# Kernel tuning notes

Measured on AMD Instinct MI355X. Metric: run time of the kernel, lower is better.

## Reference

```python
import jax, jax.numpy as jnp
import numpy as np

EPS = 1e-5
COMMIT_W = 2.0
LATENT = 64


def _conv1d(x, w, b, stride, padding):
    # x: [B,C,T], w: [O,I,K] (torch Conv1d layout)
    y = jax.lax.conv_general_dilated(x, w, (stride,), [(padding, padding)],
                                     dimension_numbers=('NCH', 'OIH', 'NCH'))
    return y + b[None, :, None]


def _bn(x, g, b):
    # training-mode BatchNorm1d: batch statistics over (B, T) per channel
    mu = x.mean(axis=(0, 2), keepdims=True)
    var = x.var(axis=(0, 2), keepdims=True)
    return (x - mu) * jax.lax.rsqrt(var + EPS) * g[None, :, None] + b[None, :, None]


def setup_inputs():
    key = jax.random.key(0)
    ks = jax.random.split(key, 10)
    B, T, D, K = 8, 10240, LATENT, 8192
    f32 = jnp.float32
    def n(k, shape, scale):
        return jax.random.normal(k, shape, dtype=f32) * scale
    return {
        'x': jax.random.normal(ks[0], (B, 1, T), dtype=f32),
        'enc_w1': n(ks[1], (16, 1, 5), 0.3), 'enc_b1': jnp.zeros((16,), f32),
        'bn1_g': jnp.ones((16,), f32), 'bn1_b': jnp.zeros((16,), f32),
        'enc_w2': n(ks[2], (32, 16, 5), 0.1), 'enc_b2': jnp.zeros((32,), f32),
        'bn2_g': jnp.ones((32,), f32), 'bn2_b': jnp.zeros((32,), f32),
        'enc_w3': n(ks[3], (64, 32, 25), 0.05), 'enc_b3': jnp.zeros((64,), f32),
        'bn3_g': jnp.ones((64,), f32), 'bn3_b': jnp.zeros((64,), f32),
        'codebook': jax.random.normal(ks[4], (K, D), dtype=f32),
        'dec_wt': n(ks[5], (64, 64, 25), 0.05),  # torch ConvTranspose1d [in,out,k]
        'dbn1_g': jnp.ones((64,), f32), 'dbn1_b': jnp.zeros((64,), f32),
        'dec_w2': n(ks[6], (64, 64, 5), 0.08), 'dec_b2': jnp.zeros((64,), f32),
        'dbn2_g': jnp.ones((64,), f32), 'dbn2_b': jnp.zeros((64,), f32),
        'dec_w3': n(ks[7], (1, 64, 1), 0.1), 'dec_b3': jnp.zeros((1,), f32),
    }


def reference(x, enc_w1, enc_b1, bn1_g, bn1_b, enc_w2, enc_b2, bn2_g, bn2_b,
              enc_w3, enc_b3, bn3_g, bn3_b, codebook, dec_wt, dbn1_g, dbn1_b,
              dec_w2, dec_b2, dbn2_g, dbn2_b, dec_w3, dec_b3):
    # ---- encoder ----
    h = jax.nn.silu(_conv1d(x, enc_w1, enc_b1, 1, 2))
    h = _bn(h, bn1_g, bn1_b)
    h = jax.nn.silu(_conv1d(h, enc_w2, enc_b2, 1, 2))
    h = _bn(h, bn2_g, bn2_b)
    h = jnp.tanh(_conv1d(h, enc_w3, enc_b3, 5, 12))
    z = _bn(h, bn3_g, bn3_b)                       # [B, 64, L]
    B, _, L = z.shape
    # ---- VQ: euclidean nearest-neighbor against codebook ----
    zf = z.transpose(0, 2, 1).reshape(-1, LATENT)  # [N, D]
    d = ((zf * zf).sum(-1, keepdims=True)
         - 2.0 * zf @ codebook.T
         + (codebook * codebook).sum(-1)[None, :])  # [N, K]
    idx = jnp.argmin(d, axis=-1)                   # [N]
    q = codebook[idx]                              # [N, D]
    commit_loss = COMMIT_W * jnp.mean((jax.lax.stop_gradient(q) - zf) ** 2)
    q_st = zf + jax.lax.stop_gradient(q - zf)      # straight-through
    zq = q_st.reshape(B, L, LATENT).transpose(0, 2, 1)  # [B, 64, L]
    # ---- decoder ----
    # ConvTranspose1d(k=25, s=5, p=12) == dilated conv with flipped kernel
    wconv = jnp.flip(dec_wt, -1).transpose(1, 0, 2)     # [out, in, k]
    h = jax.lax.conv_general_dilated(zq, wconv, (1,), [(12, 12)], lhs_dilation=(5,),
                                     dimension_numbers=('NCH', 'OIH', 'NCH'))
    h = jax.nn.silu(h)
    h = _bn(h, dbn1_g, dbn1_b)
    h = jax.nn.silu(_conv1d(h, dec_w2, dec_b2, 1, 2))
    h = _bn(h, dbn2_g, dbn2_b)
    recon = _conv1d(h, dec_w3, dec_b3, 1, 0)       # [B, 1, ~T]
    T = x.shape[2]
    cur = recon.shape[2]
    if cur > T:
        recon = recon[:, :, :T]
    elif cur < T:
        recon = jnp.pad(recon, ((0, 0), (0, 0), (0, T - cur)))
    return recon, idx.reshape(B, L), commit_loss
```

## Files before the change

kernel.cpp:

```cpp
#include <hip/hip_runtime.h>
#include <hip/hip_bf16.h>

#define DEV __device__ __forceinline__

typedef __attribute__((ext_vector_type(8))) short s8v;
typedef __attribute__((ext_vector_type(16))) float f32x16;
typedef __attribute__((address_space(1))) const unsigned int u32g;
typedef __attribute__((address_space(3))) unsigned int u32l;

DEV void gl_lds(const void* g, void* l){
  __builtin_amdgcn_global_load_lds((u32g*)g, (u32l*)l, 16, 0, 0);
}

DEV float siluf(float x){ return x / (1.f + expf(-x)); }

DEV float wredsum(float v){
  #pragma unroll
  for(int m = 32; m; m >>= 1) v += __shfl_xor(v, m);
  return v;
}

DEV unsigned short bf16rne(float f){
  unsigned int u = __float_as_uint(f);
  u += 0x7FFFu + ((u >> 16) & 1u);
  return (unsigned short)(u >> 16);
}
DEV float bf16tof(unsigned short h){ return __uint_as_float(((unsigned int)h) << 16); }

DEV unsigned umed3(unsigned a, unsigned b, unsigned c){
  unsigned d;
  asm("v_med3_u32 %0, %1, %2, %3" : "=v"(d) : "v"(a), "v"(b), "v"(c));
  return d;
}

#define S1 0
#define Q1 16
#define S2 32
#define Q2 64
#define S3 96
#define Q3 160
#define S4 224
#define Q4 288
#define S5 352
#define Q5 416
#define SLOSS 480
#define NSTATF 512

#define EPSQ 6u
#define NCHUNK 8

__global__ void k_prep(const float* dwt, unsigned short* wb7){
  const int n2 = 64*64*25;
  for(int j = blockIdx.x*blockDim.x + threadIdx.x; j < n2; j += gridDim.x*blockDim.x){
    int ii = j/(64*25), r = j - ii*(64*25), o = r/25, k = r - o*25;
    wb7[((size_t)(k*64 + o))*64 + ii] = bf16rne(dwt[j]);
  }
}

__global__ void k_prep2(const float* __restrict__ cb, unsigned short* __restrict__ cbsw,
                        float* __restrict__ cnw, float* __restrict__ cnw2,
                        unsigned short* __restrict__ cbb, int* cnt){
  if(blockIdx.x == 0 && threadIdx.x == 0) *cnt = 0;
  int j = blockIdx.x*256 + threadIdx.x;
  if(j < 8192){
    float nrm = 0.f;
    unsigned swz = (j & 15) << 4;
    char* rowp = (char*)cbsw + (size_t)j*256;
    #pragma unroll
    for(int k = 0; k < 64; k++){
      float x = cb[(size_t)j*64 + k];
      unsigned short hi = bf16rne(x);
      float lo = x - bf16tof(hi);
      *(unsigned short*)(rowp + (((unsigned)(2*k)) ^ swz)) = hi;
      *(unsigned short*)(rowp + (((unsigned)(128 + 2*k)) ^ swz)) = bf16rne(lo);
      cbb[(size_t)j*64 + k] = hi;
      nrm = fmaf(x, x, nrm);
    }
    cnw[j] = nrm;
    cnw2[j] = (nrm + 1024.f) * 256.f;
  }
}

__global__ void k1(const float* __restrict__ x, const float* __restrict__ w1,
                   const float* __restrict__ b1, float* __restrict__ h1, float* stats){
  __shared__ float xs[136];
  __shared__ float ssum[16], ssq[16];
  int tid = threadIdx.x, b = blockIdx.y, t0 = blockIdx.x*128;
  if(tid < 16){ ssum[tid] = 0.f; ssq[tid] = 0.f; }
  for(int i = tid; i < 132; i += 256){
    int t = t0 + i - 2;
    xs[i] = (t >= 0 && t < 10240) ? x[b*10240 + t] : 0.f;
  }
  __syncthreads();
  int c = tid & 15, sgrp = tid >> 4;
  float w[5];
  #pragma unroll
  for(int k = 0; k < 5; k++) w[k] = w1[c*5 + k];
  float bias = b1[c];
  float outv[8];
  float ps = 0.f, pq = 0.f;
  #pragma unroll
  for(int s = 0; s < 8; s++){
    float a = bias;
    #pragma unroll
    for(int k = 0; k < 5; k++) a = fmaf(w[k], xs[sgrp*8 + s + k], a);
    a = siluf(a);
    outv[s] = a;
    ps += a; pq += a*a;
  }
  float* op = h1 + ((size_t)(b*16 + c))*10240 + t0 + sgrp*8;
  #pragma unroll
  for(int q = 0; q < 2; q++)
    *(float4*)(op + q*4) = make_float4(outv[q*4], outv[q*4+1], outv[q*4+2], outv[q*4+3]);
  ps += __shfl_xor(ps, 16); pq += __shfl_xor(pq, 16);
  ps += __shfl_xor(ps, 32); pq += __shfl_xor(pq, 32);
  if((tid & 48) == 0){ atomicAdd(&ssum[c], ps); atomicAdd(&ssq[c], pq); }
  __syncthreads();
  if(tid < 16){ atomicAdd(stats+S1+tid, ssum[tid]); atomicAdd(stats+Q1+tid, ssq[tid]); }
}

__global__ __launch_bounds__(256) void k2(const float* __restrict__ h1,
                   const float* __restrict__ w2, const float* __restrict__ b2,
                   const float* __restrict__ g1, const float* __restrict__ bb1,
                   float* __restrict__ h2out, float* stats){
  __shared__ float hs[16][136];
  __shared__ float A1s[16], B1s[16];
  __shared__ float ssum[32], ssq[32];
  int tid = threadIdx.x, b = blockIdx.y, t0 = blockIdx.x*128;
  if(tid < 16){
    float mu = stats[S1+tid]/81920.f;
    float var = stats[Q1+tid]/81920.f - mu*mu;
    float rs = rsqrtf(var + 1e-5f);
    A1s[tid] = rs*g1[tid];
    B1s[tid] = bb1[tid] - mu*rs*g1[tid];
  }
  if(tid < 32){ ssum[tid] = 0.f; ssq[tid] = 0.f; }
  __syncthreads();
  {
    int ch = tid >> 4, j0 = tid & 15;
    float A = A1s[ch], B = B1s[ch];
    const float* hp = h1 + ((size_t)(b*16 + ch))*10240;
    for(int j = j0; j < 132; j += 16){
      int t = t0 + j - 2;
      hs[ch][j] = (t >= 0 && t < 10240) ? hp[t]*A + B : 0.f;
    }
  }
  __syncthreads();
  int c = tid & 31, tgrp = tid >> 5;
  int tb = tgrp*16;
  float acc[16];
  float bias = b2[c];
  #pragma unroll
  for(int s = 0; s < 16; s++) acc[s] = bias;
  for(int ic = 0; ic < 4; ic++){
    float wf[20];
    const float* wp = w2 + c*80 + ic*20;
    #pragma unroll
    for(int q = 0; q < 5; q++) *(float4*)(wf + q*4) = *(const float4*)(wp + q*4);
    #pragma unroll
    for(int di = 0; di < 4; di++){
      int i = ic*4 + di;
      float z[20];
      #pragma unroll
      for(int q = 0; q < 5; q++) *(float4*)(z + q*4) = *(const float4*)(&hs[i][tb] + q*4);
      float w0 = wf[di*5], w1 = wf[di*5+1], w2v = wf[di*5+2], w3 = wf[di*5+3], w4 = wf[di*5+4];
      #pragma unroll
      for(int s = 0; s < 16; s++)
        acc[s] = fmaf(w0, z[s], fmaf(w1, z[s+1], fmaf(w2v, z[s+2],
                 fmaf(w3, z[s+3], fmaf(w4, z[s+4], acc[s])))));
    }
  }
  float ps = 0.f, pq = 0.f;
  #pragma unroll
  for(int s = 0; s < 16; s++){
    float a = siluf(acc[s]);
    acc[s] = a;
    ps += a; pq += a*a;
  }
  float* op = h2out + ((size_t)(b*32 + c))*10240 + t0 + tb;
  #pragma unroll
  for(int q = 0; q < 4; q++)
    *(float4*)(op + q*4) = make_float4(acc[q*4], acc[q*4+1], acc[q*4+2], acc[q*4+3]);
  ps += __shfl_xor(ps, 32); pq += __shfl_xor(pq, 32);
  if((tid & 32) == 0){ atomicAdd(&ssum[c], ps); atomicAdd(&ssq[c], pq); }
  __syncthreads();
  if(tid < 32){ atomicAdd(stats+S2+tid, ssum[tid]); atomicAdd(stats+Q2+tid, ssq[tid]); }
}

__global__ void k3w(const float* __restrict__ ew3, const float* __restrict__ eb3,
                    const float* __restrict__ g2, const float* __restrict__ bb2,
                    const float* __restrict__ stats, float* __restrict__ w3f8,
                    float* __restrict__ cbias, float* __restrict__ zpad){
  __shared__ float A2[32], B2[32];
  __shared__ float red[256];
  int tid = threadIdx.x;
  if(tid < 32){
    float mu = stats[S2+tid]/81920.f;
    float var = stats[Q2+tid]/81920.f - mu*mu;
    float rs = rsqrtf(var + 1e-5f);
    A2[tid] = rs*g2[tid];
    B2[tid] = bb2[tid] - mu*rs*g2[tid];
  }
  __syncthreads();
  if(blockIdx.x < 200){
    int e = blockIdx.x*256 + tid;
    int kap = e % 5; int r = e / 5;
    int c = r & 63; r >>= 6;
    int kk = r % 5; int i = r / 5;
    float w = ew3[c*800 + i*25 + kap*5 + kk];
    w3f8[(((size_t)(i*5 + kk))*64 + c)*8 + kap] = w * A2[i];
  } else {
    if(tid < 32){
      float a = A2[tid];
      zpad[tid] = (fabsf(a) > 1e-30f) ? (-B2[tid] / a) : 0.f;
    }
    int c = tid & 63, ig = tid >> 6;
    float s = 0.f;
    for(int i = ig*8; i < ig*8 + 8; i++){
      float wsum = 0.f;
      #pragma unroll
      for(int k = 0; k < 25; k++) wsum += ew3[c*800 + i*25 + k];
      s += wsum * B2[i];
    }
    red[tid] = s;
    __syncthreads();
    if(tid < 64) cbias[tid] = eb3[tid] + red[tid] + red[tid+64] + red[tid+128] + red[tid+192];
  }
}

__global__ __launch_bounds__(256) void k3(const float* __restrict__ h2,
                   const float* __restrict__ w3f8, const float* __restrict__ cbias,
                   const float* __restrict__ zpad,
                   float* __restrict__ zn, float* stats){
  __shared__ float ssum[64], ssq[64];
  int tid = threadIdx.x, b = blockIdx.y, l0 = blockIdx.x*32;
  if(tid < 64){ ssum[tid] = 0.f; ssq[tid] = 0.f; }
  __syncthreads();
  int c = tid & 63, lslot = tid >> 6;
  int tbase = 5*(l0 + lslot*8) - 12;
  bool edge = (blockIdx.x == 0) || (blockIdx.x == 63);
  float acc[8];
  float cb0 = cbias[c];
  #pragma unroll
  for(int s = 0; s < 8; s++) acc[s] = cb0;
  for(int i = 0; i < 32; i++){
    const float* hp = h2 + ((size_t)(b*32 + i))*10240;
    float z[60];
    if(edge){
      float zp_i = zpad[i];
      #pragma unroll
      for(int e = 0; e < 60; e++){
        int t = tbase + e;
        z[e] = (t >= 0 && t < 10240) ? hp[t] : zp_i;
      }
    } else {
      #pragma unroll
      for(int q = 0; q < 15; q++)
        *(float4*)(z + q*4) = *(const float4*)(hp + tbase + q*4);
    }
    #pragma unroll
    for(int kk = 0; kk < 5; kk++){
      const float* wp = w3f8 + (((size_t)(i*5 + kk))*64 + c)*8;
      float w[5];
      *(float4*)w = *(const float4*)wp;
      w[4] = wp[4];
      #pragma unroll
      for(int kap = 0; kap < 5; kap++){
        #pragma unroll
        for(int s = 0; s < 8; s++)
          acc[s] = fmaf(w[kap], z[5*(s+kap) + kk], acc[s]);
      }
    }
  }
  float ls = 0.f, lq = 0.f;
  #pragma unroll
  for(int s = 0; s < 8; s++){
    int l = l0 + lslot*8 + s;
    float a = tanhf(acc[s]);
    zn[((b*2048 + l)*64) + c] = a;
    ls += a; lq += a*a;
  }
  atomicAdd(&ssum[c], ls); atomicAdd(&ssq[c], lq);
  __syncthreads();
  if(tid < 64){ atomicAdd(stats+S3+tid, ssum[tid]); atomicAdd(stats+Q3+tid, ssq[tid]); }
}

__global__ __launch_bounds__(256, 4) void k5m(const float* __restrict__ zn,
    const unsigned short* __restrict__ cbsw, const float* __restrict__ cnw2,
    const float* __restrict__ g3, const float* __restrict__ b3,
    const float* __restrict__ stats,
    unsigned int* __restrict__ pbk, unsigned int* __restrict__ psk){
  __shared__ __align__(16) unsigned char cbuf[2][16384];
  __shared__ float A3s[64], B3s[64];
  int tid = threadIdx.x;
  int chunk = blockIdx.x;
  int m0 = blockIdx.y * 128;
  int lane = tid & 63, wr = tid >> 6;
  int h = lane >> 5, cll = lane & 31;
  int row = m0 + wr*32 + cll;

  if(tid < 64){
    float mu = stats[S3+tid]/16384.f;
    float var = stats[Q3+tid]/16384.f - mu*mu;
    float rs = rsqrtf(var + 1e-5f);
    A3s[tid] = rs*g3[tid];
    B3s[tid] = b3[tid] - mu*rs*g3[tid];
  }

  int c0 = chunk * 1024;
  const char* csrc = (const char*)cbsw + (size_t)c0*256;
  #pragma unroll
  for(int c2 = 0; c2 < 4; c2++)
    gl_lds(csrc + c2*4096 + tid*16, &cbuf[0][0] + c2*4096 + tid*16);
  __syncthreads();

  s8v ah[4], al[4];
  const float* zp = zn + (size_t)row*64;
  #pragma unroll
  for(int s = 0; s < 4; s++){
    int koff = s*16 + h*8;
    float4 v0 = *(const float4*)(zp + koff);
    float4 v1 = *(const float4*)(zp + koff + 4);
    float vv[8] = {v0.x,v0.y,v0.z,v0.w,v1.x,v1.y,v1.z,v1.w};
    #pragma unroll
    for(int i = 0; i < 8; i++){
      float v = fmaf(vv[i], A3s[koff + i], B3s[koff + i]);
      unsigned short hi = bf16rne(v);
      ah[s][i] = (short)hi;
      al[s][i] = (short)bf16rne(v - bf16tof(hi));
    }
  }

  unsigned int bk[16], sk[16];
  #pragma unroll
  for(int r = 0; r < 16; r++){ bk[r] = 0xFFFFFFFFu; sk[r] = 0xFFFFFFFFu; }
  f32x16 zv;
  #pragma unroll
  for(int i = 0; i < 16; i++) zv[i] = 0.f;

  unsigned swz = (unsigned)(cll & 15) << 4;
  for(int tile = 0; tile < 16; ++tile){
    int bsel = tile & 1;
    if(tile < 15){
      const char* ns = csrc + (size_t)(tile+1)*16384;
      #pragma unroll
      for(int c2 = 0; c2 < 4; c2++)
        gl_lds(ns + c2*4096 + tid*16, &cbuf[bsel^1][0] + c2*4096 + tid*16);
    }
    #pragma unroll
    for(int half = 0; half < 2; half++){
      const unsigned char* bp = &cbuf[bsel][0] + (half*32 + cll)*256;
      s8v bh[4], bl[4];
      #pragma unroll
      for(int s = 0; s < 4; s++){
        bh[s] = *(const s8v*)(bp + (((unsigned)(s*32 + h*16)) ^ swz));
        bl[s] = *(const s8v*)(bp + (((unsigned)(128 + s*32 + h*16)) ^ swz));
      }
      unsigned col = (unsigned)(c0 + tile*64 + half*32 + cll);
      float cnv2 = cnw2[col];
      f32x16 a = __builtin_amdgcn_mfma_f32_32x32x16_bf16(ah[0], bl[0], zv, 0, 0, 0);
      a = __builtin_amdgcn_mfma_f32_32x32x16_bf16(al[0], bh[0], a, 0, 0, 0);
      a = __builtin_amdgcn_mfma_f32_32x32x16_bf16(ah[0], bh[0], a, 0, 0, 0);
      #pragma unroll
      for(int s = 1; s < 4; s++){
        a = __builtin_amdgcn_mfma_f32_32x32x16_bf16(ah[s], bl[s], a, 0, 0, 0);
        a = __builtin_amdgcn_mfma_f32_32x32x16_bf16(al[s], bh[s], a, 0, 0, 0);
        a = __builtin_amdgcn_mfma_f32_32x32x16_bf16(ah[s], bh[s], a, 0, 0, 0);
      }
      #pragma unroll
      for(int r = 0; r < 16; r++){
        float q = fmaf(-512.f, a[r], cnv2);
        q = fminf(q, 524287.f);
        unsigned k = (((unsigned)q) << 13) | col;
        unsigned nb = bk[r] < k ? bk[r] : k;
        sk[r] = umed3(sk[r], bk[r], k);
        bk[r] = nb;
      }
    }
    __syncthreads();
  }

  #pragma unroll
  for(int m = 1; m <= 16; m <<= 1){
    #pragma unroll
    for(int r = 0; r < 16; r++){
      unsigned int ob = (unsigned int)__shfl_xor((int)bk[r], m);
      unsigned int os = (unsigned int)__shfl_xor((int)sk[r], m);
      unsigned int s2 = sk[r] < os ? sk[r] : os;
      sk[r] = umed3(s2, bk[r], ob);
      bk[r] = bk[r] < ob ? bk[r] : ob;
    }
  }
  if(cll == 0){
    size_t base = (size_t)chunk*16384 + m0 + wr*32 + 4*h;
    #pragma unroll
    for(int r = 0; r < 16; r++){
      int lr = (r&3) + 8*(r>>2);
      pbk[base + lr] = bk[r];
      psk[base + lr] = sk[r];
    }
  }
}

__global__ void k5r(const unsigned int* __restrict__ pbk,
                    const unsigned int* __restrict__ psk, int* __restrict__ idxw,
                    float* __restrict__ out_idx, int* __restrict__ list, int* cnt){
  int row = blockIdx.x*256 + threadIdx.x;
  unsigned int bk = pbk[row], sk = psk[row];
  #pragma unroll
  for(int c = 1; c < NCHUNK; c++){
    unsigned int ob = pbk[(size_t)c*16384 + row];
    unsigned int os = psk[(size_t)c*16384 + row];
    unsigned int s2 = sk < os ? sk : os;
    sk = umed3(s2, bk, ob);
    bk = bk < ob ? bk : ob;
  }
  int idx = (int)(bk & 0x1FFFu);
  idxw[row] = idx;
  out_idx[row] = (float)idx;
  if((sk >> 13) - (bk >> 13) <= EPSQ){
    int p = atomicAdd(cnt, 1);
    list[p] = row;
  }
}

__global__ __launch_bounds__(256) void k5x(const float* __restrict__ zn,
    const float* __restrict__ cb, const float* __restrict__ cnw,
    const float* __restrict__ g3, const float* __restrict__ b3,
    const float* __restrict__ stats,
    const int* __restrict__ list, const int* cnt,
    float* __restrict__ pxd, int* __restrict__ pxi){
  __shared__ float A3s[64], B3s[64];
  int tid = threadIdx.x;
  if(tid < 64){
    float mu = stats[S3+tid]/16384.f;
    float var = stats[Q3+tid]/16384.f - mu*mu;
    float rs = rsqrtf(var + 1e-5f);
    A3s[tid] = rs*g3[tid];
    B3s[tid] = b3[tid] - mu*rs*g3[tid];
  }
  __syncthreads();
  int chunk = blockIdx.x;
  int n = *cnt;
  int rgrp = tid >> 6, cs = tid & 63;
  int c0 = chunk * 1024;
  for(int bat = blockIdx.y; bat*4 < n; bat += 256){
    int e = bat*4 + rgrp;
    int ec = e < n ? e : n-1;
    int row = list[ec];
    float4 zr[16];
    const float4* zp = (const float4*)(zn + (size_t)row*64);
    #pragma unroll
    for(int q = 0; q < 16; q++){
      float4 v = zp[q];
      v.x = fmaf(v.x, A3s[q*4+0], B3s[q*4+0]);
      v.y = fmaf(v.y, A3s[q*4+1], B3s[q*4+1]);
      v.z = fmaf(v.z, A3s[q*4+2], B3s[q*4+2]);
      v.w = fmaf(v.w, A3s[q*4+3], B3s[q*4+3]);
      zr[q] = v;
    }
    float bd = 3.4e38f; int bi = 0;
    for(int step = 0; step < 16; step++){
      int j = c0 + step*64 + cs;
      const float4* cp = (const float4*)(cb + (size_t)j*64);
      float cnv = cnw[j];
      float da = 0.f, db = 0.f;
      #pragma unroll
      for(int q = 0; q < 16; q += 2){
        float4 ca = cp[q], cb4 = cp[q+1];
        da = fmaf(ca.x, zr[q].x, da);  da = fmaf(ca.y, zr[q].y, da);
        da = fmaf(ca.z, zr[q].z, da);  da = fmaf(ca.w, zr[q].w, da);
        db = fmaf(cb4.x, zr[q+1].x, db); db = fmaf(cb4.y, zr[q+1].y, db);
        db = fmaf(cb4.z, zr[q+1].z, db); db = fmaf(cb4.w, zr[q+1].w, db);
      }
      float d = fmaf(-2.f, da + db, cnv);
      if(d < bd){ bd = d; bi = j; }
    }
    #pragma unroll
    for(int m = 1; m <= 32; m <<= 1){
      float od = __shfl_xor(bd, m);
      int   oi = __shfl_xor(bi, m);
      if(od < bd || (od == bd && oi < bi)){ bd = od; bi = oi; }
    }
    if(cs == 0 && e < n){
      pxd[(size_t)chunk*16384 + e] = bd;
      pxi[(size_t)chunk*16384 + e] = bi;
    }
  }
}

__global__ void k5x2(const float* __restrict__ pxd, const int* __restrict__ pxi,
                     const int* __restrict__ list, const int* cnt,
                     int* __restrict__ idxw, float* __restrict__ out_idx){
  int e = blockIdx.x*256 + threadIdx.x;
  int n = *cnt;
  if(e >= n) return;
  float bd = pxd[e]; int bi = pxi[e];
  #pragma unroll
  for(int c = 1; c < NCHUNK; c++){
    float od = pxd[(size_t)c*16384 + e];
    int   oi = pxi[(size_t)c*16384 + e];
    if(od < bd || (od == bd && oi < bi)){ bd = od; bi = oi; }
  }
  int row = list[e];
  idxw[row] = bi;
  out_idx[row] = (float)bi;
}

__global__ void k_loss(const float* __restrict__ zn, const float* __restrict__ cb,
                       const float* __restrict__ g3, const float* __restrict__ b3,
                       const int* __restrict__ idxw, float* stats){
  __shared__ float A3s[64], B3s[64];
  int tid = threadIdx.x;
  if(tid < 64){
    float mu = stats[S3+tid]/16384.f;
    float var = stats[Q3+tid]/16384.f - mu*mu;
    float rs = rsqrtf(var + 1e-5f);
    A3s[tid] = rs*g3[tid];
    B3s[tid] = b3[tid] - mu*rs*g3[tid];
  }
  __syncthreads();
  int row = blockIdx.x*256 + tid;
  int code = idxw[row];
  const float* cp = cb + (size_t)code*64;
  const float* zp = zn + (size_t)row*64;
  float s = 0.f;
  #pragma unroll
  for(int k = 0; k < 64; k++){
    float v = fmaf(zp[k], A3s[k], B3s[k]);
    float dd = cp[k] - v;
    s = fmaf(dd, dd, s);
  }
  float tot = wredsum(s);
  if((tid & 63) == 0) atomicAdd(stats + SLOSS, tot);
}

__global__ __launch_bounds__(320) void k7m(const int* __restrict__ idxp,
    const unsigned short* __restrict__ cbb, const unsigned short* __restrict__ wb7,
    unsigned short* __restrict__ h4t, float* stats){
  __shared__ __align__(16) unsigned char lA[37*128];
  __shared__ float tb[5*64*33];
  __shared__ float ssum[64], ssq[64];
  int tid = threadIdx.x, b = blockIdx.y, u0 = blockIdx.x*32;
  if(tid < 64){ ssum[tid] = 0.f; ssq[tid] = 0.f; }
  {
    int m = tid >> 3, part = tid & 7;
    if(m < 37){
      int u = u0 - 2 + m;
      uint4 val = make_uint4(0,0,0,0);
      if(u >= 0 && u < 2048){
        int code = idxp[b*2048 + u];
        val = *(const uint4*)((const char*)cbb + (size_t)code*128 + part*16);
      }
      *(uint4*)(lA + m*128 + (((unsigned)(part*16)) ^ (((unsigned)m & 7) << 4))) = val;
    }
  }
  __syncthreads();
  int lane = tid & 63, h = lane >> 5, cl = lane & 31;
  int v = tid >> 6;
  const int km[5]  = {2,3,4,0,1};
  const int ovv[5] = {2,2,2,3,3};
  f32x16 acc0, acc1;
  #pragma unroll
  for(int i = 0; i < 16; i++){ acc0[i] = 0.f; acc1[i] = 0.f; }
  #pragma unroll
  for(int r = 0; r < 5; r++){
    int off = ovv[v] - r + 2;
    int m = cl + off;
    unsigned aswz = ((unsigned)m & 7) << 4;
    int k = km[v] + 5*r;
    const char* b0p = (const char*)wb7 + (size_t)(k*64 + cl)*128;
    const char* b1p = b0p + 32*128;
    #pragma unroll
    for(int s = 0; s < 4; s++){
      unsigned o = (unsigned)(s*32 + h*16);
      s8v a  = *(const s8v*)(lA + m*128 + (o ^ aswz));
      s8v b0 = *(const s8v*)(b0p + o);
      s8v b1 = *(const s8v*)(b1p + o);
      acc0 = __builtin_amdgcn_mfma_f32_32x32x16_bf16(a, b0, acc0, 0, 0, 0);
      acc1 = __builtin_amdgcn_mfma_f32_32x32x16_bf16(a, b1, acc1, 0, 0, 0);
    }
  }
  float ps0 = 0.f, pq0 = 0.f, ps1 = 0.f, pq1 = 0.f;
  #pragma unroll
  for(int r = 0; r < 16; r++){
    int ul = (r&3) + 8*(r>>2) + 4*h;
    int u = u0 + ul;
    float v0 = siluf(acc0[r]), v1 = siluf(acc1[r]);
    tb[(v*64 + cl)*33 + ul]      = v0;
    tb[(v*64 + 32 + cl)*33 + ul] = v1;
    if(v == 0 || u < 2047){ ps0 += v0; pq0 += v0*v0; ps1 += v1; pq1 += v1*v1; }
  }
  atomicAdd(&ssum[cl], ps0);      atomicAdd(&ssq[cl], pq0);
  atomicAdd(&ssum[32 + cl], ps1); atomicAdd(&ssq[32 + cl], pq1);
  __syncthreads();
  if(tid < 64){ atomicAdd(stats+S4+tid, ssum[tid]); atomicAdd(stats+Q4+tid, ssq[tid]); }
  #pragma unroll
  for(int j = 0; j < 16; j++){
    int flat = j*320 + tid;
    int tl = flat >> 5;
    int chp = flat & 31;
    int t = u0*5 + tl;
    if(t < 10236){
      int vv = tl % 5, ul = tl / 5;
      float f0 = tb[(vv*64 + 2*chp)*33 + ul];
      float f1 = tb[(vv*64 + 2*chp + 1)*33 + ul];
      unsigned int pk = (unsigned int)bf16rne(f0) | ((unsigned int)bf16rne(f1) << 16);
      size_t rowb = ((size_t)b*10248 + 2 + t)*128;
      *(unsigned int*)((char*)h4t + rowb + (((unsigned)(4*chp)) ^ (((unsigned)t & 7) << 4))) = pk;
    }
  }
}

__global__ void k8w(const float* __restrict__ w2d, const float* __restrict__ b2d,
                    const float* __restrict__ g4, const float* __restrict__ bb4,
                    const float* __restrict__ stats, unsigned short* __restrict__ wbt,
                    float* __restrict__ beta, unsigned int* __restrict__ h4tz){
  __shared__ float A4[64], B4[64];
  int tid = threadIdx.x;
  for(int i = tid; i < 3072; i += 256){
    int b = i / 384, r = i - b*384;
    int row12 = r >> 5, word = r & 31;
    int row = row12 < 2 ? row12 : 10236 + row12;
    h4tz[((size_t)b*10248 + row)*32 + word] = 0u;
  }
  if(tid < 64){
    float mu = stats[S4+tid]/81888.f;
    float var = stats[Q4+tid]/81888.f - mu*mu;
    float rs = rsqrtf(var + 1e-5f);
    A4[tid] = rs*g4[tid];
    B4[tid] = bb4[tid] - mu*rs*g4[tid];
  }
  __syncthreads();
  for(int e = tid; e < 64*64*5; e += 256){
    int c = e/320, r = e - c*320, i = r/5, k = r - i*5;
    unsigned short hw = bf16rne(w2d[e] * A4[i]);
    int row = k*64 + c;
    *(unsigned short*)((char*)wbt + (size_t)row*128 + (((unsigned)(2*i)) ^ (((unsigned)c & 7) << 4))) = hw;
  }
  if(tid < 64){
    float s = b2d[tid];
    for(int i = 0; i < 64; i++){
      float wsum = 0.f;
      #pragma unroll
      for(int k = 0; k < 5; k++) wsum += w2d[(tid*64 + i)*5 + k];
      s += wsum * B4[i];
    }
    beta[tid] = s;
  }
}

__global__ __launch_bounds__(256) void k8(const unsigned short* __restrict__ h4t,
    const unsigned short* __restrict__ wbt, const float* __restrict__ beta,
    unsigned short* __restrict__ h5b, float* stats){
  __shared__ __align__(16) unsigned char lA[68*128];
  __shared__ float ssum[64], ssq[64];
  int tid = threadIdx.x, b = blockIdx.y, t0 = blockIdx.x*64;
  if(tid < 64){ ssum[tid] = 0.f; ssq[tid] = 0.f; }
  const char* srcA = (const char*)h4t + ((size_t)b*10248 + t0)*128;
  #pragma unroll
  for(int c2 = 0; c2 < 2; c2++)
    gl_lds(srcA + c2*4096 + tid*16, lA + c2*4096 + tid*16);
  if(tid < 32) gl_lds(srcA + 8192 + tid*16, lA + 8192 + tid*16);
  __syncthreads();

  int lane = tid & 63, h = lane >> 5, cl = lane & 31;
  int widx = tid >> 6;
  int wt0 = (widx >> 1) * 32;
  int wch = (widx & 1) * 32;
  f32x16 acc;
  #pragma unroll
  for(int i = 0; i < 16; i++) acc[i] = 0.f;
  unsigned bswz = (unsigned)(cl & 7) << 4;
  #pragma unroll
  for(int k = 0; k < 5; k++){
    int l = wt0 + cl + k;
    unsigned aswz = (unsigned)((l + 6) & 7) << 4;
    const char* bp = (const char*)wbt + (size_t)(k*64 + wch + cl)*128;
    #pragma unroll
    for(int s = 0; s < 4; s++){
      unsigned o = (unsigned)(s*32 + h*16);
      s8v a  = *(const s8v*)(lA + l*128 + (o ^ aswz));
      s8v bb = *(const s8v*)(bp + (o ^ bswz));
      acc = __builtin_amdgcn_mfma_f32_32x32x16_bf16(a, bb, acc, 0, 0, 0);
    }
  }
  float bet = beta[wch + cl];
  float ps = 0.f, pq = 0.f;
  #pragma unroll
  for(int r = 0; r < 16; r++){
    int t = t0 + wt0 + (r&3) + 8*(r>>2) + 4*h;
    float v0 = siluf(acc[r] + bet);
    if(t < 10236){
      h5b[((size_t)b*10240 + t)*64 + wch + cl] = bf16rne(v0);
      ps += v0; pq += v0*v0;
    }
  }
  atomicAdd(&ssum[wch + cl], ps); atomicAdd(&ssq[wch + cl], pq);
  __syncthreads();
  if(tid < 64){ atomicAdd(stats+S5+tid, ssum[tid]); atomicAdd(stats+Q5+tid, ssq[tid]); }
}

__global__ void k9(const unsigned short* __restrict__ h5b, const float* __restrict__ w3,
                   const float* __restrict__ b3, const float* __restrict__ g5,
                   const float* __restrict__ bb5, const float* stats,
                   float* __restrict__ out){
  __shared__ float WA[64], WB[64];
  int tid = threadIdx.x;
  if(blockIdx.x == 0 && blockIdx.y == 0 && tid == 0)
    out[98304] = 2.f * stats[SLOSS] / 1048576.f;
  if(tid < 64){
    float mu = stats[S5+tid]/81888.f;
    float var = stats[Q5+tid]/81888.f - mu*mu;
    float rs = rsqrtf(var + 1e-5f);
    float A = rs*g5[tid], B = bb5[tid] - mu*rs*g5[tid];
    float w = w3[tid];
    WA[tid] = w*A; WB[tid] = w*B;
  }
  __syncthreads();
  int b = blockIdx.y;
  int t = blockIdx.x*256 + tid;
  float acc = b3[0];
  if(t < 10236){
    const unsigned short* hp = h5b + ((size_t)b*10240 + t)*64;
    #pragma unroll
    for(int q = 0; q < 8; q++){
      uint4 u = *(const uint4*)(hp + q*8);
      unsigned int ua[4] = {u.x, u.y, u.z, u.w};
      #pragma unroll
      for(int w = 0; w < 4; w++){
        int c = q*8 + w*2;
        acc += WA[c]*bf16tof((unsigned short)(ua[w] & 0xFFFFu)) + WB[c];
        acc += WA[c+1]*bf16tof((unsigned short)(ua[w] >> 16)) + WB[c+1];
      }
    }
  } else acc = 0.f;
  out[b*10240 + t] = acc;
}

extern "C" void kernel_launch(void* const* d_in, const int* in_sizes, int n_in,
                              void* d_out, int out_size, void* d_ws, size_t ws_size,
                              hipStream_t stream){
  const float* x   = (const float*)d_in[0];
  const float* ew1 = (const float*)d_in[1];
  const float* eb1 = (const float*)d_in[2];
  const float* g1  = (const float*)d_in[3];
  const float* bb1 = (const float*)d_in[4];
  const float* ew2 = (const float*)d_in[5];
  const float* eb2 = (const float*)d_in[6];
  const float* g2  = (const float*)d_in[7];
  const float* bb2 = (const float*)d_in[8];
  const float* ew3 = (const float*)d_in[9];
  const float* eb3 = (const float*)d_in[10];
  const float* g3  = (const float*)d_in[11];
  const float* bb3 = (const float*)d_in[12];
  const float* cb  = (const float*)d_in[13];
  const float* dwt = (const float*)d_in[14];
  const float* g4  = (const float*)d_in[15];
  const float* bb4 = (const float*)d_in[16];
  const float* w2d = (const float*)d_in[17];
  const float* b2d = (const float*)d_in[18];
  const float* g5  = (const float*)d_in[19];
  const float* bb5 = (const float*)d_in[20];
  const float* w3d = (const float*)d_in[21];
  const float* b3d = (const float*)d_in[22];

  char* ws = (char*)d_ws;
  float* h1   = (float*)(ws + 0);
  unsigned short* cbsw = (unsigned short*)(ws + 0);
  float* cnw  = (float*)(ws + 2097152);
  float* cnw2 = (float*)(ws + 2129920);
  float* h2   = (float*)(ws + 5242880);
  float* zn   = (float*)(ws + 15728640);
  unsigned short* h4t = (unsigned short*)(ws + 0);
  unsigned short* h5b = (unsigned short*)(ws + 20971520);
  int*   list = (int*)  (ws + 20971520);
  int*   cnt  = (int*)  (ws + 21037056);
  unsigned int* pbk = (unsigned int*)(ws + 21037312);
  unsigned int* psk = (unsigned int*)(ws + 21561600);
  float* pxd  = (float*)(ws + 22085888);
  int*   pxi  = (int*)  (ws + 22610176);
  unsigned short* wbt = (unsigned short*)(ws + 31457280);
  float* beta = (float*)(ws + 31498240);
  unsigned short* wb7 = (unsigned short*)(ws + 32000000);
  unsigned short* cbb = (unsigned short*)(ws + 32300032);
  float* w3f8 = (float*)(ws + 33400000);
  float* cbias= (float*)(ws + 42139648);
  float* zpad = (float*)(ws + 42139904);
  int*   idxw = (int*)  (ws + 42549248);
  float* stats= (float*)(ws + 42614784);
  if(ws_size < 42616832) return;

  float* out = (float*)d_out;

  hipMemsetAsync(stats, 0, NSTATF*4, stream);
  k_prep<<<400, 256, 0, stream>>>(dwt, wb7);
  k1<<<dim3(80,8), 256, 0, stream>>>(x, ew1, eb1, h1, stats);
  k2<<<dim3(80,8), 256, 0, stream>>>(h1, ew2, eb2, g1, bb1, h2, stats);
  k_prep2<<<32, 256, 0, stream>>>(cb, cbsw, cnw, cnw2, cbb, cnt);
  k3w<<<201, 256, 0, stream>>>(ew3, eb3, g2, bb2, stats, w3f8, cbias, zpad);
  k3<<<dim3(64,8), 256, 0, stream>>>(h2, w3f8, cbias, zpad, zn, stats);
  k5m<<<dim3(NCHUNK,128), 256, 0, stream>>>(zn, cbsw, cnw2, g3, bb3, stats, pbk, psk);
  k5r<<<64, 256, 0, stream>>>(pbk, psk, idxw, out + 81920, list, cnt);
  k5x<<<dim3(NCHUNK,256), 256, 0, stream>>>(zn, cb, cnw, g3, bb3, stats, list, cnt, pxd, pxi);
  k5x2<<<64, 256, 0, stream>>>(pxd, pxi, list, cnt, idxw, out + 81920);
  k_loss<<<64, 256, 0, stream>>>(zn, cb, g3, bb3, idxw, stats);
  k7m<<<dim3(64,8), 320, 0, stream>>>(idxw, cbb, wb7, h4t, stats);
  k8w<<<1, 256, 0, stream>>>(w2d, b2d, g4, bb4, stats, wbt, beta, (unsigned int*)h4t);
  k8<<<dim3(160,8), 256, 0, stream>>>(h4t, wbt, beta, h5b, stats);
  k9<<<dim3(40,8), 256, 0, stream>>>(h5b, w3d, b3d, g5, bb5, stats, out);
}
```

Measured before the change: 383.7 us.

## Pre-split strided conv3 input into polyphase padded planes and double k3 grid

Adds a k3t kernel that rewrites h2 into five stride-5 phase planes with the padding value already filled in. The strided conv k3 can then read contiguous float4 vectors per tap and drop its edge branch. k3 now computes 4 outputs per thread instead of 8 on a 128x8 grid, which cuts registers and raises parallelism. The cost is an extra launch and an extra pass over roughly 10 MB of memory. The cnt counter moves into the stats buffer, which is zeroed by the existing memset, because h2p now overlaps cnt's old location.

Result: slower. 450.1 us (+17.3%).

```diff
diff --git a/kernel.cpp b/kernel.cpp
--- a/kernel.cpp
+++ b/kernel.cpp
@@ -44,6 +44,7 @@
 #define S5 352
 #define Q5 416
 #define SLOSS 480
+#define CNTOFF 500
 #define NSTATF 512
 
 #define EPSQ 6u
@@ -59,8 +60,7 @@
 
 __global__ void k_prep2(const float* __restrict__ cb, unsigned short* __restrict__ cbsw,
                         float* __restrict__ cnw, float* __restrict__ cnw2,
-                        unsigned short* __restrict__ cbb, int* cnt){
-  if(blockIdx.x == 0 && threadIdx.x == 0) *cnt = 0;
+                        unsigned short* __restrict__ cbb){
   int j = blockIdx.x*256 + threadIdx.x;
   if(j < 8192){
     float nrm = 0.f;
@@ -228,38 +228,41 @@
   }
 }
 
-__global__ __launch_bounds__(256) void k3(const float* __restrict__ h2,
+__global__ void k3t(const float* __restrict__ h2, const float* __restrict__ zpad,
+                    float* __restrict__ h2p){
+  int row = blockIdx.x;
+  int kk = row >> 8;
+  int r  = row & 255;
+  int b  = r >> 5, i = r & 31;
+  float zp = zpad[i];
+  const float* hp = h2 + ((size_t)(b*32 + i))*10240;
+  float* op = h2p + (size_t)row*2056;
+  for(int m = threadIdx.x; m < 2056; m += 256){
+    int t = 5*m + kk - 12;
+    op[m] = (t >= 0 && t < 10240) ? hp[t] : zp;
+  }
+}
+
+__global__ __launch_bounds__(256) void k3(const float* __restrict__ h2p,
                    const float* __restrict__ w3f8, const float* __restrict__ cbias,
-                   const float* __restrict__ zpad,
                    float* __restrict__ zn, float* stats){
   __shared__ float ssum[64], ssq[64];
-  int tid = threadIdx.x, b = blockIdx.y, l0 = blockIdx.x*32;
+  int tid = threadIdx.x, b = blockIdx.y, l0 = blockIdx.x*16;
   if(tid < 64){ ssum[tid] = 0.f; ssq[tid] = 0.f; }
   __syncthreads();
   int c = tid & 63, lslot = tid >> 6;
-  int tbase = 5*(l0 + lslot*8) - 12;
-  bool edge = (blockIdx.x == 0) || (blockIdx.x == 63);
-  float acc[8];
+  int m0 = l0 + lslot*4;
+  float acc[4];
   float cb0 = cbias[c];
   #pragma unroll
-  for(int s = 0; s < 8; s++) acc[s] = cb0;
+  for(int s = 0; s < 4; s++) acc[s] = cb0;
   for(int i = 0; i < 32; i++){
-    const float* hp = h2 + ((size_t)(b*32 + i))*10240;
-    float z[60];
-    if(edge){
-      float zp_i = zpad[i];
-      #pragma unroll
-      for(int e = 0; e < 60; e++){
-        int t = tbase + e;
-        z[e] = (t >= 0 && t < 10240) ? hp[t] : zp_i;
-      }
-    } else {
-      #pragma unroll
-      for(int q = 0; q < 15; q++)
-        *(float4*)(z + q*4) = *(const float4*)(hp + tbase + q*4);
-    }
     #pragma unroll
     for(int kk = 0; kk < 5; kk++){
+      const float* xp = h2p + ((size_t)((kk*8 + b)*32 + i))*2056 + m0;
+      float z[8];
+      *(float4*)(z)     = *(const float4*)(xp);
+      *(float4*)(z + 4) = *(const float4*)(xp + 4);
       const float* wp = w3f8 + (((size_t)(i*5 + kk))*64 + c)*8;
       float w[5];
       *(float4*)w = *(const float4*)wp;
@@ -267,15 +270,15 @@
       #pragma unroll
       for(int kap = 0; kap < 5; kap++){
         #pragma unroll
-        for(int s = 0; s < 8; s++)
-          acc[s] = fmaf(w[kap], z[5*(s+kap) + kk], acc[s]);
+        for(int s = 0; s < 4; s++)
+          acc[s] = fmaf(w[kap], z[s + kap], acc[s]);
       }
     }
   }
   float ls = 0.f, lq = 0.f;
   #pragma unroll
-  for(int s = 0; s < 8; s++){
-    int l = l0 + lslot*8 + s;
+  for(int s = 0; s < 4; s++){
+    int l = l0 + lslot*4 + s;
     float a = tanhf(acc[s]);
     zn[((b*2048 + l)*64) + c] = a;
     ls += a; lq += a*a;
@@ -773,9 +776,9 @@
   float* h2   = (float*)(ws + 5242880);
   float* zn   = (float*)(ws + 15728640);
   unsigned short* h4t = (unsigned short*)(ws + 0);
+  float* h2p  = (float*)(ws + 20971520);
   unsigned short* h5b = (unsigned short*)(ws + 20971520);
   int*   list = (int*)  (ws + 20971520);
-  int*   cnt  = (int*)  (ws + 21037056);
   unsigned int* pbk = (unsigned int*)(ws + 21037312);
   unsigned int* psk = (unsigned int*)(ws + 21561600);
   float* pxd  = (float*)(ws + 22085888);
@@ -789,6 +792,7 @@
   float* zpad = (float*)(ws + 42139904);
   int*   idxw = (int*)  (ws + 42549248);
   float* stats= (float*)(ws + 42614784);
+  int*   cnt  = (int*)(stats + CNTOFF);
   if(ws_size < 42616832) return;
 
   float* out = (float*)d_out;
@@ -797,9 +801,10 @@
   k_prep<<<400, 256, 0, stream>>>(dwt, wb7);
   k1<<<dim3(80,8), 256, 0, stream>>>(x, ew1, eb1, h1, stats);
   k2<<<dim3(80,8), 256, 0, stream>>>(h1, ew2, eb2, g1, bb1, h2, stats);
-  k_prep2<<<32, 256, 0, stream>>>(cb, cbsw, cnw, cnw2, cbb, cnt);
+  k_prep2<<<32, 256, 0, stream>>>(cb, cbsw, cnw, cnw2, cbb);
   k3w<<<201, 256, 0, stream>>>(ew3, eb3, g2, bb2, stats, w3f8, cbias, zpad);
-  k3<<<dim3(64,8), 256, 0, stream>>>(h2, w3f8, cbias, zpad, zn, stats);
+  k3t<<<1280, 256, 0, stream>>>(h2, zpad, h2p);
+  k3<<<dim3(128,8), 256, 0, stream>>>(h2p, w3f8, cbias, zn, stats);
   k5m<<<dim3(NCHUNK,128), 256, 0, stream>>>(zn, cbsw, cnw2, g3, bb3, stats, pbk, psk);
   k5r<<<64, 256, 0, stream>>>(pbk, psk, idxw, out + 81920, list, cnt);
   k5x<<<dim3(NCHUNK,256), 256, 0, stream>>>(zn, cb, cnw, g3, bb3, stats, list, cnt, pxd, pxi);
```
